# Kernel optimization log

Hardware: AMD Instinct MI355X
Metric: run time of the kernel (lower is better)

Reference implementation:

```python
import jax, jax.numpy as jnp
import numpy as np

TOP_K = 2
NUM_EXPERTS = 64
AUX_COEF = 0.01


def setup_inputs() -> dict:
    key = jax.random.key(0)
    kx, kw = jax.random.split(key)
    B, S, D, E = 4, 4096, 2048, NUM_EXPERTS
    x = jax.random.normal(kx, (B, S, D), dtype=jnp.float32)
    # nn.Linear default init ~ U(-1/sqrt(D), 1/sqrt(D))
    W = jax.random.uniform(kw, (E, D), dtype=jnp.float32,
                           minval=-1.0 / np.sqrt(D), maxval=1.0 / np.sqrt(D))
    return {"x": x, "W": W}


def reference(x, W):
    B, S, D = x.shape
    E = W.shape[0]
    # router projection (no bias)
    logits = jnp.einsum('bsd,ed->bse', x, W)          # [B,S,E]
    probs = jax.nn.softmax(logits, axis=-1)           # [B,S,E]
    top_k_gates, top_k_indices = jax.lax.top_k(probs, TOP_K)  # [B,S,K]
    top_k_gates = top_k_gates / (jnp.sum(top_k_gates, axis=-1, keepdims=True) + 1e-9)
    # aux loss: fraction of routed slots per expert (one-hot mean) x mean router prob
    total_slots = B * S * TOP_K
    counts = jnp.zeros((E,), dtype=jnp.float32).at[top_k_indices.reshape(-1)].add(1.0)
    avg_tokens_per_expert = counts / total_slots      # == one_hot(idx).mean(dims 0,1,2)
    avg_router_prob = jnp.mean(probs, axis=(0, 1))    # [E]
    aux_loss = AUX_COEF * E * jnp.sum(avg_tokens_per_expert * avg_router_prob)
    return top_k_indices, top_k_gates, aux_loss
```

## Files before the change

### kernel.cpp

```cpp
#include <hip/hip_runtime.h>
#include <math.h>

#define NTOK 16384
#define DDIM 2048
#define NEXP 64
#define TMB  64
#define NBLK (NTOK / TMB)
#define NCH  32
#define NS   64

typedef _Float16 half8v __attribute__((ext_vector_type(8)));
typedef float    f32x4  __attribute__((ext_vector_type(4)));

#define MFMA16(a, b, c) __builtin_amdgcn_mfma_f32_16x16x32_f16((a), (b), (c), 0, 0, 0)

__device__ __forceinline__ void cvt8(float4 a, float4 b, half8v& h, half8v& l) {
    h[0]=(_Float16)a.x; l[0]=(_Float16)(a.x-(float)h[0]);
    h[1]=(_Float16)a.y; l[1]=(_Float16)(a.y-(float)h[1]);
    h[2]=(_Float16)a.z; l[2]=(_Float16)(a.z-(float)h[2]);
    h[3]=(_Float16)a.w; l[3]=(_Float16)(a.w-(float)h[3]);
    h[4]=(_Float16)b.x; l[4]=(_Float16)(b.x-(float)h[4]);
    h[5]=(_Float16)b.y; l[5]=(_Float16)(b.y-(float)h[5]);
    h[6]=(_Float16)b.z; l[6]=(_Float16)(b.z-(float)h[6]);
    h[7]=(_Float16)b.w; l[7]=(_Float16)(b.w-(float)h[7]);
}

__global__ __launch_bounds__(256, 1) void router_kernel(
    const float* __restrict__ x, const float* __restrict__ W,
    float* __restrict__ accg, float* __restrict__ out)
{
    __shared__ __align__(16) _Float16 Ah[2][4096];
    __shared__ __align__(16) _Float16 Al[2][4096];
    __shared__ float lgt[TMB][NEXP + 1];
    __shared__ float cnt[NEXP];
    __shared__ int lastBlk;

    const int tid  = threadIdx.x;
    const int lane = tid & 63;
    const int wv   = __builtin_amdgcn_readfirstlane(tid >> 6);
    const int m0   = blockIdx.x * TMB;

    if (tid < NEXP) cnt[tid] = 0.0f;

    const int r    = tid >> 2;
    const int c0   = (tid & 3) * 16;
    const int tile = r >> 4, tok = r & 15;
    const int S0 = c0 >> 5,       q0 = (c0 >> 3) & 3;
    const int S1 = (c0+8) >> 5,   q1 = ((c0+8) >> 3) & 3;
    const int g0 = S0*64 + q0*16 + tok,  g1 = S1*64 + q1*16 + tok;
    const int off0 = tile*1024 + (g0 ^ ((g0>>4)&7)) * 8;
    const int off1 = tile*1024 + (g1 ^ ((g1>>4)&7)) * 8;

    const float* gx = x + (size_t)(m0 + r) * DDIM + c0;

    const int gr1 = 64 + lane;
    const int rd0 = (lane ^ ((lane>>4)&7)) * 8;
    const int rd1 = (gr1 ^ ((gr1>>4)&7)) * 8;

    const float* wfp = W + (size_t)(wv * 16 + (lane & 15)) * DDIM + (lane >> 4) * 8;

    f32x4 acc0 = {0.f,0.f,0.f,0.f}, acc1 = {0.f,0.f,0.f,0.f};
    f32x4 acc2 = {0.f,0.f,0.f,0.f}, acc3 = {0.f,0.f,0.f,0.f};

    float4 xa0 = *(const float4*)(gx +  0), xa1 = *(const float4*)(gx +  4);
    float4 xa2 = *(const float4*)(gx +  8), xa3 = *(const float4*)(gx + 12);
    float4 xb0 = *(const float4*)(gx + 64), xb1 = *(const float4*)(gx + 68);
    float4 xb2 = *(const float4*)(gx + 72), xb3 = *(const float4*)(gx + 76);
    float4 w0a = *(const float4*)(wfp +  0), w0b = *(const float4*)(wfp +  4);
    float4 w1a = *(const float4*)(wfp + 32), w1b = *(const float4*)(wfp + 36);
    float4 w2a = *(const float4*)(wfp + 64), w2b = *(const float4*)(wfp + 68);
    float4 w3a = *(const float4*)(wfp + 96), w3b = *(const float4*)(wfp + 100);

#define STEPBODY(RD, BH, BL)                                                 \
    {                                                                        \
        half8v a0h = *(const half8v*)&Ah[PB_][   0 + RD];                    \
        half8v a0l = *(const half8v*)&Al[PB_][   0 + RD];                    \
        half8v a1h = *(const half8v*)&Ah[PB_][1024 + RD];                    \
        half8v a1l = *(const half8v*)&Al[PB_][1024 + RD];                    \
        half8v a2h = *(const half8v*)&Ah[PB_][2048 + RD];                    \
        half8v a2l = *(const half8v*)&Al[PB_][2048 + RD];                    \
        half8v a3h = *(const half8v*)&Ah[PB_][3072 + RD];                    \
        half8v a3l = *(const half8v*)&Al[PB_][3072 + RD];                    \
        acc0 = MFMA16(a0l, BH, acc0);                                        \
        acc0 = MFMA16(a0h, BL, acc0);                                        \
        acc0 = MFMA16(a0h, BH, acc0);                                        \
        acc1 = MFMA16(a1l, BH, acc1);                                        \
        acc1 = MFMA16(a1h, BL, acc1);                                        \
        acc1 = MFMA16(a1h, BH, acc1);                                        \
        acc2 = MFMA16(a2l, BH, acc2);                                        \
        acc2 = MFMA16(a2h, BL, acc2);                                        \
        acc2 = MFMA16(a2h, BH, acc2);                                        \
        acc3 = MFMA16(a3l, BH, acc3);                                        \
        acc3 = MFMA16(a3h, BL, acc3);                                        \
        acc3 = MFMA16(a3h, BH, acc3);                                        \
    }

#define CHUNK(ch, X0, X1, X2, X3, PB, WAa, WAb, WBa, WBb)                   \
    {                                                                        \
        const int PB_ = (PB);                                                \
        half8v h_, l_;                                                       \
        cvt8(X0, X1, h_, l_);                                                \
        *(half8v*)&Ah[PB_][off0] = h_;  *(half8v*)&Al[PB_][off0] = l_;       \
        cvt8(X2, X3, h_, l_);                                                \
        *(half8v*)&Ah[PB_][off1] = h_;  *(half8v*)&Al[PB_][off1] = l_;       \
        const int cf = ((ch) + 2 < NCH) ? (ch) + 2 : 0;                      \
        X0 = *(const float4*)(gx + cf * 64 +  0);                            \
        X1 = *(const float4*)(gx + cf * 64 +  4);                            \
        X2 = *(const float4*)(gx + cf * 64 +  8);                            \
        X3 = *(const float4*)(gx + cf * 64 + 12);                            \
        __builtin_amdgcn_sched_barrier(0);       \
        asm volatile("s_waitcnt lgkmcnt(0)" ::: "memory");                   \
        __builtin_amdgcn_s_barrier();                                        \
        __builtin_amdgcn_sched_barrier(0);   \
        {                                                \
            half8v bh, bl;                                                   \
            cvt8(WAa, WAb, bh, bl);                                          \
            const int SgN = (2 * (ch) + 4) & (NS - 1);                       \
            WAa = *(const float4*)(wfp + SgN * 32);                          \
            WAb = *(const float4*)(wfp + SgN * 32 + 4);                      \
            STEPBODY(rd0, bh, bl)                                            \
        }                                                                    \
        {                                              \
            half8v bh, bl;                                                   \
            cvt8(WBa, WBb, bh, bl);                                          \
            const int SgN = (2 * (ch) + 5) & (NS - 1);                       \
            WBa = *(const float4*)(wfp + SgN * 32);                          \
            WBb = *(const float4*)(wfp + SgN * 32 + 4);                      \
            STEPBODY(rd1, bh, bl)                                            \
        }                                                                    \
    }

    for (int cb = 0; cb < NCH; cb += 2) {
        CHUNK(cb + 0, xa0, xa1, xa2, xa3, 0, w0a, w0b, w1a, w1b);
        CHUNK(cb + 1, xb0, xb1, xb2, xb3, 1, w2a, w2b, w3a, w3b);
    }
#undef CHUNK
#undef STEPBODY

    {
        const int qr = lane >> 4;
        const int nl = lane & 15;
        #pragma unroll
        for (int rr = 0; rr < 4; ++rr) {
            const int mm = qr * 4 + rr;
            lgt[ 0 + mm][wv * 16 + nl] = acc0[rr];
            lgt[16 + mm][wv * 16 + nl] = acc1[rr];
            lgt[32 + mm][wv * 16 + nl] = acc2[rr];
            lgt[48 + mm][wv * 16 + nl] = acc3[rr];
        }
    }
    __syncthreads();

    for (int pass = 0; pass < 2; ++pass) {
        const int m = pass * 32 + (tid >> 3);
        const int j = tid & 7;
        float l[8];
        #pragma unroll
        for (int i = 0; i < 8; ++i) l[i] = lgt[m][j * 8 + i];

        float mx = l[0];
        #pragma unroll
        for (int i = 1; i < 8; ++i) mx = fmaxf(mx, l[i]);
        #pragma unroll
        for (int off = 1; off < 8; off <<= 1) mx = fmaxf(mx, __shfl_xor(mx, off, 8));

        float ev[8];
        float zs = 0.f;
        float v1 = -INFINITY, v2 = -INFINITY;
        int i1 = 0, i2 = 0;
        #pragma unroll
        for (int i = 0; i < 8; ++i) {
            ev[i] = __expf(l[i] - mx);
            zs += ev[i];
            int e = j * 8 + i;
            if (l[i] > v1)      { v2 = v1; i2 = i1; v1 = l[i]; i1 = e; }
            else if (l[i] > v2) { v2 = l[i]; i2 = e; }
        }
        #pragma unroll
        for (int off = 1; off < 8; off <<= 1) zs += __shfl_xor(zs, off, 8);

        #pragma unroll
        for (int off = 1; off < 8; off <<= 1) {
            float ov1 = __shfl_xor(v1, off, 8);
            int   oi1 = __shfl_xor(i1, off, 8);
            float ov2 = __shfl_xor(v2, off, 8);
            int   oi2 = __shfl_xor(i2, off, 8);
            bool afirst = (v1 > ov1) || (v1 == ov1 && i1 < oi1);
            if (afirst) {
                bool t = (v2 > ov1) || (v2 == ov1 && i2 < oi1);
                v2 = t ? v2 : ov1;
                i2 = t ? i2 : oi1;
            } else {
                bool t = (ov2 > v1) || (ov2 == v1 && oi2 < i1);
                v2 = t ? ov2 : v1;
                i2 = t ? oi2 : i1;
                v1 = ov1;
                i1 = oi1;
            }
        }

        const float invz = 1.0f / zs;
        if (j == 0) {
            float p1 = invz;
            float p2 = __expf(v2 - mx) * invz;
            float sden = p1 + p2 + 1e-9f;
            int tokg = m0 + m;
            out[tokg * 2 + 0] = (float)i1;
            out[tokg * 2 + 1] = (float)i2;
            out[32768 + tokg * 2 + 0] = p1 / sden;
            out[32768 + tokg * 2 + 1] = p2 / sden;
            atomicAdd(&cnt[i1], 1.0f);
            atomicAdd(&cnt[i2], 1.0f);
        }

        #pragma unroll
        for (int i = 0; i < 8; ++i) lgt[m][j * 8 + i] = ev[i] * invz;
    }
    __syncthreads();

    if (tid < NEXP) {
        atomicAdd(&accg[tid], cnt[tid]);
    } else if (tid < 128) {
        int e = tid - 64;
        float s = 0.f;
        #pragma unroll
        for (int t = 0; t < TMB; ++t) s += lgt[t][e];
        atomicAdd(&accg[64 + e], s);
    }
    __syncthreads();

    if (tid == 0) {
        __threadfence();
        unsigned int old = atomicAdd((unsigned int*)(accg + 128), 1u);
        lastBlk = (old == NBLK - 1) ? 1 : 0;
    }
    __syncthreads();
    if (lastBlk && tid < 64) {
        __threadfence();
        const volatile float* ag = accg;
        float c = ag[tid];
        float p = ag[64 + tid];
        float term = (c / (float)(NTOK * 2)) * (p / (float)NTOK);
        #pragma unroll
        for (int off = 1; off < 64; off <<= 1) term += __shfl_xor(term, off, 64);
        if (tid == 0) out[65536] = 0.01f * (float)NEXP * term;
    }
}

extern "C" void kernel_launch(void* const* d_in, const int* in_sizes, int n_in,
                              void* d_out, int out_size, void* d_ws, size_t ws_size,
                              hipStream_t stream) {
    const float* x = (const float*)d_in[0];
    const float* W = (const float*)d_in[1];
    float* out  = (float*)d_out;
    float* accg = (float*)d_ws;

    hipMemsetAsync(accg, 0, 1024, stream);
    router_kernel<<<NBLK, 256, 0, stream>>>(x, W, accg, out);
}
```

Baseline: 224.9 us.

## Stage fp32 x and W tiles into LDS via async global_load_lds double buffering

Replaces the register-staged path, which converted x to fp16 hi/lo halves before writing LDS and streamed W through registers, with direct global-to-LDS DMA loads (global_load_lds) of raw fp32 tiles for both x and W. Chunks are 128 wide and double-buffered with __syncthreads between them. The fp16 hi/lo split now happens after reading from LDS. The aim is to hide global memory latency and free registers and VALU from the load path. The cost is that each wave now converts all 64 token rows itself, so conversion work goes up, and the LDS footprint grows to roughly 128KB of staging buffers.

```diff
diff --git a/kernel.cpp b/kernel.cpp
--- a/kernel.cpp
+++ b/kernel.cpp
@@ -6,13 +6,19 @@
 #define NEXP 64
 #define TMB  64
 #define NBLK (NTOK / TMB)
-#define NCH  32
-#define NS   64
+#define CHF  128
+#define NCHK (DDIM / CHF)
 
 typedef _Float16 half8v __attribute__((ext_vector_type(8)));
 typedef float    f32x4  __attribute__((ext_vector_type(4)));
 
 #define MFMA16(a, b, c) __builtin_amdgcn_mfma_f32_16x16x32_f16((a), (b), (c), 0, 0, 0)
+
+__device__ __forceinline__ void stage16(const void* g, void* l) {
+    __builtin_amdgcn_global_load_lds(
+        (const __attribute__((address_space(1))) unsigned int*)g,
+        (__attribute__((address_space(3))) unsigned int*)l, 16, 0, 0);
+}
 
 __device__ __forceinline__ void cvt8(float4 a, float4 b, half8v& h, half8v& l) {
     h[0]=(_Float16)a.x; l[0]=(_Float16)(a.x-(float)h[0]);
@@ -29,8 +35,8 @@
     const float* __restrict__ x, const float* __restrict__ W,
     float* __restrict__ accg, float* __restrict__ out)
 {
-    __shared__ __align__(16) _Float16 Ah[2][4096];
-    __shared__ __align__(16) _Float16 Al[2][4096];
+    __shared__ __align__(16) float Xs[2][8192];
+    __shared__ __align__(16) float Ws[2][8192];
     __shared__ float lgt[TMB][NEXP + 1];
     __shared__ float cnt[NEXP];
     __shared__ int lastBlk;
@@ -42,100 +48,87 @@
 
     if (tid < NEXP) cnt[tid] = 0.0f;
 
-    const int r    = tid >> 2;
-    const int c0   = (tid & 3) * 16;
-    const int tile = r >> 4, tok = r & 15;
-    const int S0 = c0 >> 5,       q0 = (c0 >> 3) & 3;
-    const int S1 = (c0+8) >> 5,   q1 = ((c0+8) >> 3) & 3;
-    const int g0 = S0*64 + q0*16 + tok,  g1 = S1*64 + q1*16 + tok;
-    const int off0 = tile*1024 + (g0 ^ ((g0>>4)&7)) * 8;
-    const int off1 = tile*1024 + (g1 ^ ((g1>>4)&7)) * 8;
-
-    const float* gx = x + (size_t)(m0 + r) * DDIM + c0;
-
-    const int gr1 = 64 + lane;
-    const int rd0 = (lane ^ ((lane>>4)&7)) * 8;
-    const int rd1 = (gr1 ^ ((gr1>>4)&7)) * 8;
-
-    const float* wfp = W + (size_t)(wv * 16 + (lane & 15)) * DDIM + (lane >> 4) * 8;
+#define MKOFF(i) ({ int p_ = (i)*32 + (lane >> 1);                           \
+                    int g_ = p_ ^ ((p_ >> 4) & 7);                           \
+                    (g_ & 15)*2048 + (g_ >> 6)*32 + ((g_ >> 4) & 3)*8        \
+                    + (lane & 1)*4; })
+    const int o0 = MKOFF(0), o1 = MKOFF(1), o2 = MKOFF(2), o3 = MKOFF(3);
+    const int o4 = MKOFF(4), o5 = MKOFF(5), o6 = MKOFF(6), o7 = MKOFF(7);
+#undef MKOFF
+
+    const float* bx = x + (size_t)(m0 + wv * 16) * DDIM;
+    const float* bw = W + (size_t)(wv * 16) * DDIM;
+
+#define MKP(S) ({ int g_ = (S)*64 + ((lane >> 4) << 4) + (lane & 15);        \
+                  (g_ ^ ((g_ >> 4) & 7)) * 8; })
+    const int pf0 = MKP(0), pf1 = MKP(1), pf2 = MKP(2), pf3 = MKP(3);
+#undef MKP
 
     f32x4 acc0 = {0.f,0.f,0.f,0.f}, acc1 = {0.f,0.f,0.f,0.f};
     f32x4 acc2 = {0.f,0.f,0.f,0.f}, acc3 = {0.f,0.f,0.f,0.f};
 
-    float4 xa0 = *(const float4*)(gx +  0), xa1 = *(const float4*)(gx +  4);
-    float4 xa2 = *(const float4*)(gx +  8), xa3 = *(const float4*)(gx + 12);
-    float4 xb0 = *(const float4*)(gx + 64), xb1 = *(const float4*)(gx + 68);
-    float4 xb2 = *(const float4*)(gx + 72), xb3 = *(const float4*)(gx + 76);
-    float4 w0a = *(const float4*)(wfp +  0), w0b = *(const float4*)(wfp +  4);
-    float4 w1a = *(const float4*)(wfp + 32), w1b = *(const float4*)(wfp + 36);
-    float4 w2a = *(const float4*)(wfp + 64), w2b = *(const float4*)(wfp + 68);
-    float4 w3a = *(const float4*)(wfp + 96), w3b = *(const float4*)(wfp + 100);
-
-#define STEPBODY(RD, BH, BL)                                                 \
+#define STAGE(cc, B)                                                         \
     {                                                                        \
-        half8v a0h = *(const half8v*)&Ah[PB_][   0 + RD];                    \
-        half8v a0l = *(const half8v*)&Al[PB_][   0 + RD];                    \
-        half8v a1h = *(const half8v*)&Ah[PB_][1024 + RD];                    \
-        half8v a1l = *(const half8v*)&Al[PB_][1024 + RD];                    \
-        half8v a2h = *(const half8v*)&Ah[PB_][2048 + RD];                    \
-        half8v a2l = *(const half8v*)&Al[PB_][2048 + RD];                    \
-        half8v a3h = *(const half8v*)&Ah[PB_][3072 + RD];                    \
-        half8v a3l = *(const half8v*)&Al[PB_][3072 + RD];                    \
-        acc0 = MFMA16(a0l, BH, acc0);                                        \
-        acc0 = MFMA16(a0h, BL, acc0);                                        \
-        acc0 = MFMA16(a0h, BH, acc0);                                        \
-        acc1 = MFMA16(a1l, BH, acc1);                                        \
-        acc1 = MFMA16(a1h, BL, acc1);                                        \
-        acc1 = MFMA16(a1h, BH, acc1);                                        \
-        acc2 = MFMA16(a2l, BH, acc2);                                        \
-        acc2 = MFMA16(a2h, BL, acc2);                                        \
-        acc2 = MFMA16(a2h, BH, acc2);                                        \
-        acc3 = MFMA16(a3l, BH, acc3);                                        \
-        acc3 = MFMA16(a3h, BL, acc3);                                        \
-        acc3 = MFMA16(a3h, BH, acc3);                                        \
-    }
-
-#define CHUNK(ch, X0, X1, X2, X3, PB, WAa, WAb, WBa, WBb)                   \
+        const float* bx_ = bx + (size_t)(cc) * CHF;                          \
+        const float* bw_ = bw + (size_t)(cc) * CHF;                          \
+        float* dx_ = &Xs[B][wv * 2048];                                      \
+        float* dw_ = &Ws[B][wv * 2048];                                      \
+        stage16(bx_ + o0, dx_ +    0);  stage16(bw_ + o0, dw_ +    0);       \
+        stage16(bx_ + o1, dx_ +  256);  stage16(bw_ + o1, dw_ +  256);       \
+        stage16(bx_ + o2, dx_ +  512);  stage16(bw_ + o2, dw_ +  512);       \
+        stage16(bx_ + o3, dx_ +  768);  stage16(bw_ + o3, dw_ +  768);       \
+        stage16(bx_ + o4, dx_ + 1024);  stage16(bw_ + o4, dw_ + 1024);       \
+        stage16(bx_ + o5, dx_ + 1280);  stage16(bw_ + o5, dw_ + 1280);       \
+        stage16(bx_ + o6, dx_ + 1536);  stage16(bw_ + o6, dw_ + 1536);       \
+        stage16(bx_ + o7, dx_ + 1792);  stage16(bw_ + o7, dw_ + 1792);       \
+    }
+
+#define STEP(PB, PF)                                                         \
     {                                                                        \
-        const int PB_ = (PB);                                                \
-        half8v h_, l_;                                                       \
-        cvt8(X0, X1, h_, l_);                                                \
-        *(half8v*)&Ah[PB_][off0] = h_;  *(half8v*)&Al[PB_][off0] = l_;       \
-        cvt8(X2, X3, h_, l_);                                                \
-        *(half8v*)&Ah[PB_][off1] = h_;  *(half8v*)&Al[PB_][off1] = l_;       \
-        const int cf = ((ch) + 2 < NCH) ? (ch) + 2 : 0;                      \
-        X0 = *(const float4*)(gx + cf * 64 +  0);                            \
-        X1 = *(const float4*)(gx + cf * 64 +  4);                            \
-        X2 = *(const float4*)(gx + cf * 64 +  8);                            \
-        X3 = *(const float4*)(gx + cf * 64 + 12);                            \
-        __builtin_amdgcn_sched_barrier(0);       \
-        asm volatile("s_waitcnt lgkmcnt(0)" ::: "memory");                   \
-        __builtin_amdgcn_s_barrier();                                        \
-        __builtin_amdgcn_sched_barrier(0);   \
-        {                                                \
-            half8v bh, bl;                                                   \
-            cvt8(WAa, WAb, bh, bl);                                          \
-            const int SgN = (2 * (ch) + 4) & (NS - 1);                       \
-            WAa = *(const float4*)(wfp + SgN * 32);                          \
-            WAb = *(const float4*)(wfp + SgN * 32 + 4);                      \
-            STEPBODY(rd0, bh, bl)                                            \
-        }                                                                    \
-        {                                              \
-            half8v bh, bl;                                                   \
-            cvt8(WBa, WBb, bh, bl);                                          \
-            const int SgN = (2 * (ch) + 5) & (NS - 1);                       \
-            WBa = *(const float4*)(wfp + SgN * 32);                          \
-            WBb = *(const float4*)(wfp + SgN * 32 + 4);                      \
-            STEPBODY(rd1, bh, bl)                                            \
-        }                                                                    \
-    }
-
-    for (int cb = 0; cb < NCH; cb += 2) {
-        CHUNK(cb + 0, xa0, xa1, xa2, xa3, 0, w0a, w0b, w1a, w1b);
-        CHUNK(cb + 1, xb0, xb1, xb2, xb3, 1, w2a, w2b, w3a, w3b);
-    }
-#undef CHUNK
-#undef STEPBODY
+        float4 v0, v1;                                                       \
+        half8v bh, bl;                                                       \
+        v0 = *(const float4*)&Ws[PB][wv * 2048 + (PF)];                      \
+        v1 = *(const float4*)&Ws[PB][wv * 2048 + (PF) + 4];                  \
+        cvt8(v0, v1, bh, bl);                                                \
+        half8v a0h,a0l,a1h,a1l,a2h,a2l,a3h,a3l;                              \
+        v0 = *(const float4*)&Xs[PB][       (PF)];                           \
+        v1 = *(const float4*)&Xs[PB][       (PF) + 4];  cvt8(v0,v1,a0h,a0l); \
+        v0 = *(const float4*)&Xs[PB][2048 + (PF)];                           \
+        v1 = *(const float4*)&Xs[PB][2048 + (PF) + 4];  cvt8(v0,v1,a1h,a1l); \
+        v0 = *(const float4*)&Xs[PB][4096 + (PF)];                           \
+        v1 = *(const float4*)&Xs[PB][4096 + (PF) + 4];  cvt8(v0,v1,a2h,a2l); \
+        v0 = *(const float4*)&Xs[PB][6144 + (PF)];                           \
+        v1 = *(const float4*)&Xs[PB][6144 + (PF) + 4];  cvt8(v0,v1,a3h,a3l); \
+        acc0 = MFMA16(a0l, bh, acc0);                                        \
+        acc0 = MFMA16(a0h, bl, acc0);                                        \
+        acc0 = MFMA16(a0h, bh, acc0);                                        \
+        acc1 = MFMA16(a1l, bh, acc1);                                        \
+        acc1 = MFMA16(a1h, bl, acc1);                                        \
+        acc1 = MFMA16(a1h, bh, acc1);                                        \
+        acc2 = MFMA16(a2l, bh, acc2);                                        \
+        acc2 = MFMA16(a2h, bl, acc2);                                        \
+        acc2 = MFMA16(a2h, bh, acc2);                                        \
+        acc3 = MFMA16(a3l, bh, acc3);                                        \
+        acc3 = MFMA16(a3h, bl, acc3);                                        \
+        acc3 = MFMA16(a3h, bh, acc3);                                        \
+    }
+
+#define COMPUTE(PB)                                                          \
+    STEP(PB, pf0) STEP(PB, pf1) STEP(PB, pf2) STEP(PB, pf3)
+
+    STAGE(0, 0);
+
+    for (int cb = 0; cb < NCHK; cb += 2) {
+        __syncthreads();
+        STAGE(cb + 1, 1);
+        COMPUTE(0);
+        __syncthreads();
+        if (cb + 2 < NCHK) STAGE(cb + 2, 0);
+        COMPUTE(1);
+    }
+#undef COMPUTE
+#undef STEP
+#undef STAGE
 
     {
         const int qr = lane >> 4;
```

After: 220.7 us. About the same (-1.8%).
